# Kernel tuning notes

Hardware: AMD Instinct MI355X
Metric: run time of the kernel (lower is better)

Reference implementation:

```python
import jax, jax.numpy as jnp
import numpy as np

B, T, I, D, O = 256, 512, 64, 512, 128
LN_EPS = 1e-5


def setup_inputs() -> dict:
    key = jax.random.key(0)
    ks = jax.random.split(key, 4)
    x = jax.random.normal(ks[0], (B, T, I), dtype=jnp.float32)
    W_in = jax.random.normal(ks[1], (D, I), dtype=jnp.float32) * (1.0 / np.sqrt(I))
    b_in = jnp.zeros((D,), dtype=jnp.float32)
    gamma = jnp.ones((D,), dtype=jnp.float32)
    beta = jnp.zeros((D,), dtype=jnp.float32)
    W_out = jax.random.normal(ks[2], (O, D), dtype=jnp.float32) * (1.0 / np.sqrt(D))
    b_out = jnp.zeros((O,), dtype=jnp.float32)
    context_strength = jnp.float32(0.2)
    return {"x": x, "W_in": W_in, "b_in": b_in, "gamma": gamma, "beta": beta,
            "W_out": W_out, "b_out": b_out, "context_strength": context_strength}


def reference(x, W_in, b_in, gamma, beta, W_out, b_out, context_strength):
    # memory_ring slot 0 is the only one ever read/written, so context_read at
    # step t is simply state_update from step t-1 (zeros at t=0).
    b, t, _ = x.shape
    d = W_in.shape[0]
    # Precompute all input embeddings in one GEMM: [B,T,D]
    e = jnp.tanh(jnp.einsum('bti,di->btd', x, W_in) + b_in)
    scale = jax.nn.sigmoid(context_strength)

    def layer_norm(s):
        mu = jnp.mean(s, axis=-1, keepdims=True)
        var = jnp.mean((s - mu) ** 2, axis=-1, keepdims=True)
        return (s - mu) * jax.lax.rsqrt(var + LN_EPS) * gamma + beta

    def step(carry, e_t):
        s_prev, h_prev = carry  # state_update_{t-1}, hidden_{t-1}
        s = jnp.tanh(e_t + scale * s_prev + h_prev)
        h = layer_norm(s)
        return (s, h), None

    init = (jnp.zeros((b, d), dtype=x.dtype), jnp.zeros((b, d), dtype=x.dtype))
    (_, h_final), _ = jax.lax.scan(step, init, jnp.swapaxes(e, 0, 1))  # scan over T
    logits = h_final @ W_out.T + b_out  # [B,O]
    return logits
```

## Files before the change

kernel.cpp:

```cpp
#include <hip/hip_runtime.h>

#define BB 256
#define TT 512
#define II 64
#define DD 512
#define OO 128
#define LN_EPS 1e-5f

__device__ __forceinline__ float fast_tanh(float x) {
    float e = __expf(2.0f * x);
    return 1.0f - 2.0f / (e + 1.0f);
}

__global__ __launch_bounds__(256)
void fused_kernel(const float* __restrict__ x,
                  const float* __restrict__ W_in,
                  const float* __restrict__ b_in,
                  const float* __restrict__ gamma,
                  const float* __restrict__ beta,
                  const float* __restrict__ W_out,
                  const float* __restrict__ b_out,
                  const float* __restrict__ cs,
                  float* __restrict__ out)
{
    const int b    = blockIdx.x;
    const int tid  = threadIdx.x;
    const int wave = tid >> 6;
    const int lane = tid & 63;
    const int d2   = tid << 1;

    __shared__ __align__(16) float4 xrow[2][16];
    __shared__ __align__(16) float red[2][4][2];
    __shared__ float h_lds[DD];

    float4 wA[16], wB[16];
    {
        const float* wrA = W_in + (size_t)d2 * II;
        const float* wrB = W_in + (size_t)(d2 + 1) * II;
        #pragma unroll
        for (int k = 0; k < 16; ++k) {
            wA[k] = *(const float4*)(wrA + k * 4);
            wB[k] = *(const float4*)(wrB + k * 4);
        }
    }
    const float2 bin = *(const float2*)(b_in + d2);
    const float2 g   = *(const float2*)(gamma + d2);
    const float2 bt  = *(const float2*)(beta  + d2);
    const float scale = 1.0f / (1.0f + __expf(-cs[0]));

    const float* xb = x + (size_t)b * TT * II;

    float4 xg;
    if (tid < 16) {
        xrow[0][tid] = *(const float4*)(xb + (size_t)0 * II + tid * 4);
        xrow[1][tid] = *(const float4*)(xb + (size_t)1 * II + tid * 4);
        xg           = *(const float4*)(xb + (size_t)2 * II + tid * 4);
    }
    __syncthreads();

    float2 ecur;
    {
        float ax = 0.0f, ay = 0.0f;
        #pragma unroll
        for (int k = 0; k < 16; ++k) {
            const float4 xv = xrow[0][k];
            ax = fmaf(xv.x, wA[k].x, ax); ax = fmaf(xv.y, wA[k].y, ax);
            ax = fmaf(xv.z, wA[k].z, ax); ax = fmaf(xv.w, wA[k].w, ax);
            ay = fmaf(xv.x, wB[k].x, ay); ay = fmaf(xv.y, wB[k].y, ay);
            ay = fmaf(xv.z, wB[k].z, ay); ay = fmaf(xv.w, wB[k].w, ay);
        }
        ecur.x = fast_tanh(ax + bin.x);
        ecur.y = fast_tanh(ay + bin.y);
    }
    __syncthreads();

    float2 sp, hp;
    sp.x = sp.y = 0.0f; hp = sp;

    #pragma unroll 1
    for (int t = 0; t < TT; ++t) {
        float2 s;
        s.x = fast_tanh(ecur.x + scale * sp.x + hp.x);
        s.y = fast_tanh(ecur.y + scale * sp.y + hp.y);

        float r0 = s.x + s.y;
        float r1 = s.x * s.x + s.y * s.y;
        #pragma unroll
        for (int m = 32; m >= 1; m >>= 1) {
            r0 += __shfl_xor(r0, m, 64);
            r1 += __shfl_xor(r1, m, 64);
        }

        float2 en;
        {
            float ax = 0.0f, ay = 0.0f;
            const float4* xr = xrow[(t + 1) & 1];
            #pragma unroll
            for (int k = 0; k < 16; ++k) {
                const float4 xv = xr[k];
                ax = fmaf(xv.x, wA[k].x, ax); ax = fmaf(xv.y, wA[k].y, ax);
                ax = fmaf(xv.z, wA[k].z, ax); ax = fmaf(xv.w, wA[k].w, ax);
                ay = fmaf(xv.x, wB[k].x, ay); ay = fmaf(xv.y, wB[k].y, ay);
                ay = fmaf(xv.z, wB[k].z, ay); ay = fmaf(xv.w, wB[k].w, ay);
            }
            en.x = fast_tanh(ax + bin.x);
            en.y = fast_tanh(ay + bin.y);
        }

        const int p = t & 1;
        if (lane == 0) { red[p][wave][0] = r0; red[p][wave][1] = r1; }

        if (tid < 16) {
            xrow[t & 1][tid] = xg;
            const int tld = (t + 3 < TT) ? (t + 3) : (TT - 1);
            xg = *(const float4*)(xb + (size_t)tld * II + tid * 4);
        }
        __syncthreads();

        const float4 ra = *(const float4*)&red[p][0][0];
        const float4 rb = *(const float4*)&red[p][2][0];
        const float sum   = (ra.x + ra.z) + (rb.x + rb.z);
        const float sumsq = (ra.y + ra.w) + (rb.y + rb.w);

        const float mu   = sum * (1.0f / DD);
        const float var  = sumsq * (1.0f / DD) - mu * mu;
        const float rstd = rsqrtf(var + LN_EPS);

        hp.x = (s.x - mu) * rstd * g.x + bt.x;
        hp.y = (s.y - mu) * rstd * g.y + bt.y;
        sp = s;
        ecur = en;
    }

    h_lds[d2]     = hp.x;
    h_lds[d2 + 1] = hp.y;
    __syncthreads();

    const int dbase = lane * 8;
    float hreg[8];
    #pragma unroll
    for (int k = 0; k < 8; ++k) hreg[k] = h_lds[dbase + k];

    for (int oo = 0; oo < 32; ++oo) {
        const int o = wave * 32 + oo;
        const float* wo = W_out + (size_t)o * DD + dbase;
        float pacc = 0.f;
        #pragma unroll
        for (int k = 0; k < 8; ++k) pacc = fmaf(wo[k], hreg[k], pacc);
        #pragma unroll
        for (int m = 32; m >= 1; m >>= 1) pacc += __shfl_xor(pacc, m, 64);
        if (lane == 0) out[(size_t)b * OO + o] = pacc + b_out[o];
    }
}

extern "C" void kernel_launch(void* const* d_in, const int* in_sizes, int n_in,
                              void* d_out, int out_size, void* d_ws, size_t ws_size,
                              hipStream_t stream) {
    const float* x      = (const float*)d_in[0];
    const float* W_in   = (const float*)d_in[1];
    const float* b_in   = (const float*)d_in[2];
    const float* gamma  = (const float*)d_in[3];
    const float* beta   = (const float*)d_in[4];
    const float* W_out  = (const float*)d_in[5];
    const float* b_out  = (const float*)d_in[6];
    const float* cs     = (const float*)d_in[7];
    float* out = (float*)d_out;

    (void)d_ws; (void)ws_size;

    fused_kernel<<<BB, 256, 0, stream>>>(x, W_in, b_in, gamma, beta,
                                         W_out, b_out, cs, out);
}
```

Measured before the change: 553.0 us.

## Load x rows directly into registers instead of staging through LDS

Drops the LDS double-buffer for x rows. Every thread now loads the full 64-float x row straight from global memory (a broadcast load) into 16 float4 registers, prefetching one step ahead, and computes the next embedding after the LayerNorm update. This removes the LDS reads and writes for x and the extra synchronisation they required, at the cost of 64 more registers per thread and redundant global/L1 loads issued by all 256 threads.

```diff
diff --git a/kernel.cpp b/kernel.cpp
--- a/kernel.cpp
+++ b/kernel.cpp
@@ -29,7 +29,6 @@
     const int lane = tid & 63;
     const int d2   = tid << 1;
 
-    __shared__ __align__(16) float4 xrow[2][16];
     __shared__ __align__(16) float red[2][4][2];
     __shared__ float h_lds[DD];
 
@@ -50,20 +49,16 @@
 
     const float* xb = x + (size_t)b * TT * II;
 
-    float4 xg;
-    if (tid < 16) {
-        xrow[0][tid] = *(const float4*)(xb + (size_t)0 * II + tid * 4);
-        xrow[1][tid] = *(const float4*)(xb + (size_t)1 * II + tid * 4);
-        xg           = *(const float4*)(xb + (size_t)2 * II + tid * 4);
-    }
-    __syncthreads();
+    float4 xn[16];
+    #pragma unroll
+    for (int k = 0; k < 16; ++k) xn[k] = *(const float4*)(xb + k * 4);
 
     float2 ecur;
     {
         float ax = 0.0f, ay = 0.0f;
         #pragma unroll
         for (int k = 0; k < 16; ++k) {
-            const float4 xv = xrow[0][k];
+            const float4 xv = xn[k];
             ax = fmaf(xv.x, wA[k].x, ax); ax = fmaf(xv.y, wA[k].y, ax);
             ax = fmaf(xv.z, wA[k].z, ax); ax = fmaf(xv.w, wA[k].w, ax);
             ay = fmaf(xv.x, wB[k].x, ay); ay = fmaf(xv.y, wB[k].y, ay);
@@ -72,7 +67,9 @@
         ecur.x = fast_tanh(ax + bin.x);
         ecur.y = fast_tanh(ay + bin.y);
     }
-    __syncthreads();
+    #pragma unroll
+    for (int k = 0; k < 16; ++k)
+        xn[k] = *(const float4*)(xb + (size_t)1 * II + k * 4);
 
     float2 sp, hp;
     sp.x = sp.y = 0.0f; hp = sp;
@@ -91,30 +88,8 @@
             r1 += __shfl_xor(r1, m, 64);
         }
 
-        float2 en;
-        {
-            float ax = 0.0f, ay = 0.0f;
-            const float4* xr = xrow[(t + 1) & 1];
-            #pragma unroll
-            for (int k = 0; k < 16; ++k) {
-                const float4 xv = xr[k];
-                ax = fmaf(xv.x, wA[k].x, ax); ax = fmaf(xv.y, wA[k].y, ax);
-                ax = fmaf(xv.z, wA[k].z, ax); ax = fmaf(xv.w, wA[k].w, ax);
-                ay = fmaf(xv.x, wB[k].x, ay); ay = fmaf(xv.y, wB[k].y, ay);
-                ay = fmaf(xv.z, wB[k].z, ay); ay = fmaf(xv.w, wB[k].w, ay);
-            }
-            en.x = fast_tanh(ax + bin.x);
-            en.y = fast_tanh(ay + bin.y);
-        }
-
         const int p = t & 1;
         if (lane == 0) { red[p][wave][0] = r0; red[p][wave][1] = r1; }
-
-        if (tid < 16) {
-            xrow[t & 1][tid] = xg;
-            const int tld = (t + 3 < TT) ? (t + 3) : (TT - 1);
-            xg = *(const float4*)(xb + (size_t)tld * II + tid * 4);
-        }
         __syncthreads();
 
         const float4 ra = *(const float4*)&red[p][0][0];
@@ -129,7 +104,28 @@
         hp.x = (s.x - mu) * rstd * g.x + bt.x;
         hp.y = (s.y - mu) * rstd * g.y + bt.y;
         sp = s;
-        ecur = en;
+
+        {
+            float ax = 0.0f, ay = 0.0f;
+            #pragma unroll
+            for (int k = 0; k < 16; ++k) {
+                const float4 xv = xn[k];
+                ax = fmaf(xv.x, wA[k].x, ax); ax = fmaf(xv.y, wA[k].y, ax);
+                ax = fmaf(xv.z, wA[k].z, ax); ax = fmaf(xv.w, wA[k].w, ax);
+                ay = fmaf(xv.x, wB[k].x, ay); ay = fmaf(xv.y, wB[k].y, ay);
+                ay = fmaf(xv.z, wB[k].z, ay); ay = fmaf(xv.w, wB[k].w, ay);
+            }
+            ecur.x = fast_tanh(ax + bin.x);
+            ecur.y = fast_tanh(ay + bin.y);
+        }
+
+        {
+            const int tld = (t + 2 < TT) ? (t + 2) : (TT - 1);
+            const float* xr = xb + (size_t)tld * II;
+            #pragma unroll
+            for (int k = 0; k < 16; ++k)
+                xn[k] = *(const float4*)(xr + k * 4);
+        }
     }
 
     h_lds[d2]     = hp.x;
```

Measured after the change: 1.226 ms. +121.8%, slower.
